# Kernel optimization log

Measured on AMD Instinct MI355X. Metric: run time of the kernel, lower is better.

Reference implementation:

```python
import jax, jax.numpy as jnp
import numpy as np

LORA_RANK = 16
LORA_ALPHA = 32
CHUNK_SIZE = 256
TTT_LR = 0.01
CLIP_THRESHOLD = 1.0
SCALING = LORA_ALPHA / LORA_RANK
LN_EPS = 1e-5


def setup_inputs() -> dict:
    key = jax.random.key(0)
    ks = jax.random.split(key, 5)
    B, S, K, H = 2, 8192, 1024, 1024
    x = jax.random.normal(ks[0], (B, S, K), dtype=jnp.float32)
    Wb = jax.random.normal(ks[1], (H, K), dtype=jnp.float32) / np.sqrt(K)
    init_A = jax.random.normal(ks[2], (H, LORA_RANK), dtype=jnp.float32) * 0.01
    init_B = jax.random.normal(ks[3], (LORA_RANK, K), dtype=jnp.float32) * 0.01
    ln_gamma = jnp.ones((K,), dtype=jnp.float32)
    ln_beta = jnp.zeros((K,), dtype=jnp.float32)
    Wp = jax.random.normal(ks[4], (H, K), dtype=jnp.float32) / np.sqrt(K)
    return {"x": x, "Wb": Wb, "init_A": init_A, "init_B": init_B,
            "ln_gamma": ln_gamma, "ln_beta": ln_beta, "Wp": Wp}


def _forward(x, Wb, init_A, init_B, ln_gamma, ln_beta, Wp):
    B_sz, Seq, k_dim = x.shape
    h_dim = Wb.shape[0]
    r = init_A.shape[1]
    nc = Seq // CHUNK_SIZE  # Seq chosen divisible; pad_len == 0

    base_out = x @ Wb.T  # [B, S, H]

    # --- target construction under no_grad: LayerNorm + left-shift ---
    xd = jax.lax.stop_gradient(x)
    mu = jnp.mean(xd, axis=-1, keepdims=True)
    var = jnp.mean((xd - mu) ** 2, axis=-1, keepdims=True)
    xn = (xd - mu) * jax.lax.rsqrt(var + LN_EPS) * ln_gamma + ln_beta
    shifted = jnp.pad(xn[:, 1:, :], ((0, 0), (0, 1), (0, 0)))
    shifted = jax.lax.stop_gradient(shifted)

    V = shifted @ Wp.T  # [B, S, H]

    Z = x.reshape(B_sz * nc, CHUNK_SIZE, k_dim)
    Vc = V.reshape(B_sz * nc, CHUNK_SIZE, h_dim)

    # per-chunk fast-weight deltas
    proj_in = Z @ init_B.T                                # [BC, C, r]
    dA = jnp.einsum('bch,bcr->bhr', Vc, proj_in)          # [BC, H, r]
    proj_err = Vc @ init_A                                # [BC, C, r]
    dB = jnp.einsum('bcr,bck->brk', proj_err, Z)          # [BC, r, K]

    dA = dA.reshape(B_sz, nc, h_dim, r)
    dB = dB.reshape(B_sz, nc, r, k_dim)

    # exclusive cross-chunk cumsum
    accA = jnp.cumsum(dA, axis=1)
    accB = jnp.cumsum(dB, axis=1)
    accA = jnp.concatenate([jnp.zeros_like(accA[:, :1]), accA[:, :-1]], axis=1)
    accB = jnp.concatenate([jnp.zeros_like(accB[:, :1]), accB[:, :-1]], axis=1)

    lr = TTT_LR * SCALING
    rawA = (lr * accA).reshape(-1, h_dim, r)
    rawB = (lr * accB).reshape(-1, r, k_dim)

    # joint norm clip (norm_type=2)
    norm_sq = (jnp.sum(rawA.astype(jnp.float32) ** 2, axis=(-2, -1), keepdims=True)
               + jnp.sum(rawB.astype(jnp.float32) ** 2, axis=(-2, -1), keepdims=True))
    total_norm = jnp.sqrt(norm_sq)
    coef = jnp.minimum(CLIP_THRESHOLD / (total_norm + 1e-6), 1.0).astype(rawA.dtype)

    A_eff = init_A[None] - rawA * coef  # [BC, H, r]
    B_eff = init_B[None] - rawB * coef  # [BC, r, K]

    mid = jnp.einsum('bck,brk->bcr', Z, B_eff)          # [BC, C, r]
    lora = jnp.einsum('bcr,bhr->bch', mid, A_eff)       # [BC, C, H]
    lora = lora.reshape(B_sz, Seq, h_dim)

    return base_out + lora * SCALING


def reference(x, Wb, init_A, init_B, ln_gamma, ln_beta, Wp):
    return _forward(x, Wb, init_A, init_B, ln_gamma, ln_beta, Wp)
```

## Files before the change

### kernel.cpp

```cpp
#include <hip/hip_runtime.h>

typedef __attribute__((ext_vector_type(8))) short s16x8;
typedef __attribute__((ext_vector_type(4))) float f32x4;
typedef unsigned short u16;

#define B_SZ 2
#define SEQ 8192
#define KD 1024
#define HD 1024
#define RK 16
#define CH 256
#define NCH 64
static constexpr float LR_SC = 0.02f;
static constexpr float SCALE_OUT = 2.0f;

__device__ __forceinline__ u16 f2b(float f) {
  union { float f; unsigned int u; } c; c.f = f;
  unsigned int u = c.u;
  unsigned int r = (u + 0x7fffu + ((u >> 16) & 1u)) >> 16;
  return (u16)r;
}
__device__ __forceinline__ float b2f(u16 v) {
  union { unsigned int u; float f; } c; c.u = ((unsigned int)v) << 16; return c.f;
}
__device__ __forceinline__ void async16(const u16* g, u16* l) {
  __builtin_amdgcn_global_load_lds((const __attribute__((address_space(1))) void*)g,
                                   (__attribute__((address_space(3))) void*)l, 16, 0, 0);
}

__global__ __launch_bounds__(256) void cvt_bf16(const float* __restrict__ src,
                                                u16* __restrict__ dst, int n) {
  int i = (blockIdx.x * 256 + threadIdx.x) * 4;
  if (i < n) {
    float4 v = *(const float4*)(src + i);
    ushort4 o; o.x = f2b(v.x); o.y = f2b(v.y); o.z = f2b(v.z); o.w = f2b(v.w);
    *(ushort4*)(dst + i) = o;
  }
}

__global__ __launch_bounds__(256) void cvt_at(const float* __restrict__ A,
                                              u16* __restrict__ At) {
  int i = blockIdx.x * 256 + threadIdx.x;
  if (i < HD * RK) {
    int h = i >> 4, j = i & 15;
    At[(size_t)j * HD + h] = f2b(A[i]);
  }
}

__global__ __launch_bounds__(256) void ln_shift(const float* __restrict__ x,
                                                const float* __restrict__ gamma,
                                                const float* __restrict__ beta,
                                                u16* __restrict__ xb,
                                                u16* __restrict__ shb) {
  int row = blockIdx.x;
  int t = threadIdx.x;
  int s = row & (SEQ - 1);
  const float* xr = x + (size_t)row * KD;
  float4 v = *(const float4*)(xr + t * 4);
  ushort4 o; o.x = f2b(v.x); o.y = f2b(v.y); o.z = f2b(v.z); o.w = f2b(v.w);
  *(ushort4*)(xb + (size_t)row * KD + t * 4) = o;

  if (s == 0) {
    ushort4 z; z.x = 0; z.y = 0; z.z = 0; z.w = 0;
    *(ushort4*)(shb + ((size_t)row + SEQ - 1) * KD + t * 4) = z;
    return;
  }
  float s1 = v.x + v.y + v.z + v.w;
  float s2 = v.x * v.x + v.y * v.y + v.z * v.z + v.w * v.w;
  #pragma unroll
  for (int off = 32; off > 0; off >>= 1) {
    s1 += __shfl_down(s1, off);
    s2 += __shfl_down(s2, off);
  }
  __shared__ float red[8];
  int wave = t >> 6, lane = t & 63;
  if (lane == 0) { red[wave * 2] = s1; red[wave * 2 + 1] = s2; }
  __syncthreads();
  float sum = red[0] + red[2] + red[4] + red[6];
  float ssq = red[1] + red[3] + red[5] + red[7];
  float mu = sum * (1.0f / KD);
  float var = ssq * (1.0f / KD) - mu * mu;
  float rstd = rsqrtf(var + 1e-5f);
  float4 g = *(const float4*)(gamma + t * 4);
  float4 bb = *(const float4*)(beta + t * 4);
  ushort4 so;
  so.x = f2b((v.x - mu) * rstd * g.x + bb.x);
  so.y = f2b((v.y - mu) * rstd * g.y + bb.y);
  so.z = f2b((v.z - mu) * rstd * g.z + bb.z);
  so.w = f2b((v.w - mu) * rstd * g.w + bb.w);
  *(ushort4*)(shb + (size_t)(row - 1) * KD + t * 4) = so;
}

__global__ __launch_bounds__(256, 2) void gemm_v(const u16* __restrict__ A,
                                                 const u16* __restrict__ Bm,
                                                 u16* __restrict__ C) {
  constexpr int BM = 128, BN = 128, BK = 32, N = HD, Kd = KD;
  __shared__ u16 As[BM * BK];
  __shared__ u16 Bs[BN * BK];
  int tid = threadIdx.x;
  int lane = tid & 63, wave = tid >> 6;
  int m0 = blockIdx.y * BM, n0 = blockIdx.x * BN;
  int wm = (wave >> 1) * 64, wn = (wave & 1) * 64;
  int lr = lane & 15, lk = (lane >> 4) * 8;
  f32x4 acc[4][4] = {};

  const u16* gbase; u16* lbase;
  if (wave < 2) { gbase = A + (size_t)(m0 + wave * 64) * Kd; lbase = As + wave * 64 * BK; }
  else          { gbase = Bm + (size_t)(n0 + (wave - 2) * 64) * Kd; lbase = Bs + (wave - 2) * 64 * BK; }
  int srow = lane >> 2, scol = (lane & 3) * 8;
  const u16* gsrc = gbase + (size_t)srow * Kd + scol;

  for (int k0 = 0; k0 < Kd; k0 += BK) {
    #pragma unroll
    for (int i = 0; i < 4; i++)
      async16(gsrc + (size_t)i * 16 * Kd, lbase + i * 16 * BK);
    gsrc += BK;
    __syncthreads();
    s16x8 af[4], bfr[4];
    #pragma unroll
    for (int i = 0; i < 4; i++) af[i] = *(const s16x8*)(As + (wm + i * 16 + lr) * BK + lk);
    #pragma unroll
    for (int j = 0; j < 4; j++) bfr[j] = *(const s16x8*)(Bs + (wn + j * 16 + lr) * BK + lk);
    #pragma unroll
    for (int i = 0; i < 4; i++)
      #pragma unroll
      for (int j = 0; j < 4; j++)
        acc[i][j] = __builtin_amdgcn_mfma_f32_16x16x32_bf16(af[i], bfr[j], acc[i][j], 0, 0, 0);
    __syncthreads();
  }
  int rb = (lane >> 4) * 4, cc = lane & 15;
  #pragma unroll
  for (int i = 0; i < 4; i++)
    #pragma unroll
    for (int j = 0; j < 4; j++)
      #pragma unroll
      for (int p = 0; p < 4; p++)
        C[(size_t)(m0 + wm + i * 16 + rb + p) * N + (n0 + wn + j * 16 + cc)] = f2b(acc[i][j][p]);
}

__global__ __launch_bounds__(256, 2) void gemm_fused(const u16* __restrict__ A,
                                                     const u16* __restrict__ Bm,
                                                     const u16* __restrict__ mid2,
                                                     const u16* __restrict__ Aef,
                                                     float* __restrict__ C) {
  constexpr int BM = 128, BN = 128, BK = 32, N = HD, Kd = KD;
  __shared__ u16 As[BM * BK];
  __shared__ u16 Bs[BN * BK];
  int tid = threadIdx.x;
  int lane = tid & 63, wave = tid >> 6;
  int m0 = blockIdx.y * BM, n0 = blockIdx.x * BN;
  int wm = (wave >> 1) * 64, wn = (wave & 1) * 64;
  int lr = lane & 15, lk = (lane >> 4) * 8;
  f32x4 acc[4][4] = {};

  const u16* gbase; u16* lbase;
  if (wave < 2) { gbase = A + (size_t)(m0 + wave * 64) * Kd; lbase = As + wave * 64 * BK; }
  else          { gbase = Bm + (size_t)(n0 + (wave - 2) * 64) * Kd; lbase = Bs + (wave - 2) * 64 * BK; }
  int srow = lane >> 2, scol = (lane & 3) * 8;
  const u16* gsrc = gbase + (size_t)srow * Kd + scol;

  for (int k0 = 0; k0 < Kd; k0 += BK) {
    #pragma unroll
    for (int i = 0; i < 4; i++)
      async16(gsrc + (size_t)i * 16 * Kd, lbase + i * 16 * BK);
    gsrc += BK;
    __syncthreads();
    s16x8 af[4], bfr[4];
    #pragma unroll
    for (int i = 0; i < 4; i++) af[i] = *(const s16x8*)(As + (wm + i * 16 + lr) * BK + lk);
    #pragma unroll
    for (int j = 0; j < 4; j++) bfr[j] = *(const s16x8*)(Bs + (wn + j * 16 + lr) * BK + lk);
    #pragma unroll
    for (int i = 0; i < 4; i++)
      #pragma unroll
      for (int j = 0; j < 4; j++)
        acc[i][j] = __builtin_amdgcn_mfma_f32_16x16x32_bf16(af[i], bfr[j], acc[i][j], 0, 0, 0);
    __syncthreads();
  }

  {
    int chunk = blockIdx.y >> 1;
    const u16* mbase = mid2;
    const u16* abase = Aef + (size_t)chunk * (HD * RK);
    int klane = lane >> 4;
    s16x8 am2[4], bn2[4];
    #pragma unroll
    for (int i = 0; i < 4; i++) {
      if (klane < 2)
        am2[i] = *(const s16x8*)(mbase + (size_t)(m0 + wm + i * 16 + lr) * RK + klane * 8);
      else { s16x8 z = {}; am2[i] = z; }
    }
    #pragma unroll
    for (int j = 0; j < 4; j++) {
      if (klane < 2)
        bn2[j] = *(const s16x8*)(abase + (size_t)(n0 + wn + j * 16 + lr) * RK + klane * 8);
      else { s16x8 z = {}; bn2[j] = z; }
    }
    #pragma unroll
    for (int i = 0; i < 4; i++)
      #pragma unroll
      for (int j = 0; j < 4; j++)
        acc[i][j] = __builtin_amdgcn_mfma_f32_16x16x32_bf16(am2[i], bn2[j], acc[i][j], 0, 0, 0);
  }

  int rb = (lane >> 4) * 4, cc = lane & 15;
  #pragma unroll
  for (int i = 0; i < 4; i++)
    #pragma unroll
    for (int j = 0; j < 4; j++)
      #pragma unroll
      for (int p = 0; p < 4; p++)
        C[(size_t)(m0 + wm + i * 16 + rb + p) * N + (n0 + wn + j * 16 + cc)] = acc[i][j][p];
}

__global__ __launch_bounds__(256) void rank16_proj(const u16* __restrict__ xb,
                                                   const u16* __restrict__ Vb,
                                                   const u16* __restrict__ iBb,
                                                   const u16* __restrict__ iAt,
                                                   float* __restrict__ pin,
                                                   float* __restrict__ per) {
  const u16* X; const u16* W; float* O;
  if (blockIdx.z == 0) { X = xb; W = iBb; O = pin; }
  else                 { X = Vb; W = iAt; O = per; }
  int wave = threadIdx.x >> 6, lane = threadIdx.x & 63;
  int m0 = (blockIdx.x * 4 + wave) * 16;
  int lr = lane & 15, lk = (lane >> 4) * 8;
  const u16* xp = X + (size_t)(m0 + lr) * KD + lk;
  const u16* wp = W + (size_t)lr * KD + lk;
  f32x4 acc = {};
  #pragma unroll 4
  for (int k0 = 0; k0 < KD; k0 += 32) {
    s16x8 a = *(const s16x8*)xp;
    s16x8 b = *(const s16x8*)wp;
    acc = __builtin_amdgcn_mfma_f32_16x16x32_bf16(a, b, acc, 0, 0, 0);
    xp += 32; wp += 32;
  }
  int rb = (lane >> 4) * 4, cc = lane & 15;
  #pragma unroll
  for (int p = 0; p < 4; p++)
    O[(size_t)(m0 + rb + p) * RK + cc] = acc[p];
}

__global__ __launch_bounds__(256) void rank16_mid(const u16* __restrict__ xb,
                                                  const u16* __restrict__ Bef,
                                                  u16* __restrict__ mid2) {
  int wave = threadIdx.x >> 6, lane = threadIdx.x & 63;
  int m0 = (blockIdx.x * 4 + wave) * 16;
  int chunk = m0 >> 8;
  int lr = lane & 15, lk = (lane >> 4) * 8;
  const u16* xp = xb + (size_t)(m0 + lr) * KD + lk;
  const u16* wp = Bef + (size_t)chunk * (RK * KD) + (size_t)lr * KD + lk;
  f32x4 acc = {};
  #pragma unroll 4
  for (int k0 = 0; k0 < KD; k0 += 32) {
    s16x8 a = *(const s16x8*)xp;
    s16x8 b = *(const s16x8*)wp;
    acc = __builtin_amdgcn_mfma_f32_16x16x32_bf16(a, b, acc, 0, 0, 0);
    xp += 32; wp += 32;
  }
  int rb = (lane >> 4) * 4, cc = lane & 15;
  #pragma unroll
  for (int p = 0; p < 4; p++)
    mid2[(size_t)(m0 + rb + p) * RK + cc] = f2b(SCALE_OUT * acc[p]);
}

__global__ __launch_bounds__(256) void dadb_kernel(const u16* __restrict__ xb,
                                                   const u16* __restrict__ Vb,
                                                   const float* __restrict__ proj_in,
                                                   const float* __restrict__ proj_err,
                                                   float* __restrict__ dA,
                                                   float* __restrict__ dB) {
  int tile = blockIdx.x;
  int chunk = blockIdx.y;
  int which = blockIdx.z;
  int t = threadIdx.x;
  __shared__ float P[CH * RK];
  const float* psrc = which ? proj_err : proj_in;
  for (int i = t; i < 1024; i += 256)
    *(float4*)&P[i * 4] = *(const float4*)&psrc[(size_t)chunk * 4096 + i * 4];
  __syncthreads();
  float acc[16];
  #pragma unroll
  for (int j = 0; j < 16; j++) acc[j] = 0.f;
  int col = tile * 256 + t;
  const u16* src = which ? (xb + (size_t)chunk * CH * KD + col)
                         : (Vb + (size_t)chunk * CH * HD + col);
  for (int c = 0; c < 256; c++) {
    float v = b2f(src[(size_t)c * 1024]);
    const float4* pr = (const float4*)&P[c * 16];
    #pragma unroll
    for (int q = 0; q < 4; q++) {
      float4 p = pr[q];
      acc[q*4+0] += v * p.x; acc[q*4+1] += v * p.y;
      acc[q*4+2] += v * p.z; acc[q*4+3] += v * p.w;
    }
  }
  if (which == 0) {
    float* o = dA + (size_t)chunk * 16384 + (size_t)col * 16;
    #pragma unroll
    for (int q = 0; q < 4; q++) {
      float4 r; r.x = acc[q*4]; r.y = acc[q*4+1]; r.z = acc[q*4+2]; r.w = acc[q*4+3];
      *(float4*)&o[q * 4] = r;
    }
  } else {
    float* o = dB + (size_t)chunk * 16384 + col;
    #pragma unroll
    for (int j = 0; j < 16; j++) o[(size_t)j * 1024] = acc[j];
  }
}

__global__ __launch_bounds__(256) void cumsum_kernel(const float* __restrict__ dA,
                                                     const float* __restrict__ dB,
                                                     float* __restrict__ rawA,
                                                     float* __restrict__ rawB) {
  int idx = blockIdx.x * 256 + threadIdx.x;
  int which = idx >> 15;
  int rem = idx & 32767;
  int b = rem >> 14;
  int e = rem & 16383;
  const float* src = which ? dB : dA;
  float* dst = which ? rawB : rawA;
  size_t base = (size_t)b * 32 * 16384 + e;
  float run = 0.f;
  for (int i = 0; i < 32; i++) {
    size_t off = base + (size_t)i * 16384;
    float nv = src[off];
    dst[off] = LR_SC * run;
    run += nv;
  }
}

__global__ __launch_bounds__(256) void coef_kernel(const float* __restrict__ rawA,
                                                   const float* __restrict__ rawB,
                                                   float* __restrict__ coef) {
  int chunk = blockIdx.x, t = threadIdx.x;
  const float* a = rawA + (size_t)chunk * 16384;
  const float* b = rawB + (size_t)chunk * 16384;
  float s = 0.f;
  for (int i = t * 4; i < 16384; i += 1024) {
    float4 v = *(const float4*)(a + i);
    s += v.x*v.x + v.y*v.y + v.z*v.z + v.w*v.w;
    float4 w = *(const float4*)(b + i);
    s += w.x*w.x + w.y*w.y + w.z*w.z + w.w*w.w;
  }
  #pragma unroll
  for (int off = 32; off > 0; off >>= 1) s += __shfl_down(s, off);
  __shared__ float red[4];
  int wave = t >> 6, lane = t & 63;
  if (lane == 0) red[wave] = s;
  __syncthreads();
  if (t == 0) {
    float tot = red[0] + red[1] + red[2] + red[3];
    float n = sqrtf(tot);
    coef[chunk] = fminf(1.0f / (n + 1e-6f), 1.0f);
  }
}

__global__ __launch_bounds__(256) void eff_kernel(const float* __restrict__ initA,
                                                  const float* __restrict__ initB,
                                                  const float* __restrict__ rawA,
                                                  const float* __restrict__ rawB,
                                                  const float* __restrict__ coef,
                                                  u16* __restrict__ Aef,
                                                  u16* __restrict__ Bef) {
  int idx = blockIdx.x * 256 + threadIdx.x;
  int which = idx >> 18;
  int rem = idx & 262143;
  int chunk = rem >> 12;
  int e = (rem & 4095) * 4;
  float cf = coef[chunk];
  const float* ini = which ? initB : initA;
  const float* raw = (which ? rawB : rawA) + (size_t)chunk * 16384;
  u16* out = (which ? Bef : Aef) + (size_t)chunk * 16384;
  float4 iv = *(const float4*)(ini + e);
  float4 rv = *(const float4*)(raw + e);
  ushort4 r;
  r.x = f2b(iv.x - rv.x * cf); r.y = f2b(iv.y - rv.y * cf);
  r.z = f2b(iv.z - rv.z * cf); r.w = f2b(iv.w - rv.w * cf);
  *(ushort4*)(out + e) = r;
}

extern "C" void kernel_launch(void* const* d_in, const int* in_sizes, int n_in,
                              void* d_out, int out_size, void* d_ws, size_t ws_size,
                              hipStream_t stream) {
  (void)in_sizes; (void)n_in; (void)out_size; (void)ws_size;
  const float* x     = (const float*)d_in[0];
  const float* Wb    = (const float*)d_in[1];
  const float* initA = (const float*)d_in[2];
  const float* initB = (const float*)d_in[3];
  const float* gamma = (const float*)d_in[4];
  const float* beta  = (const float*)d_in[5];
  const float* Wp    = (const float*)d_in[6];
  float* out = (float*)d_out;

  char* ws = (char*)d_ws;
  size_t off = 0;
  auto alloc = [&](size_t bytes) -> void* {
    void* p = ws + off;
    off = (off + bytes + 255) & ~(size_t)255;
    return p;
  };
  const size_t ROWS = (size_t)B_SZ * SEQ;
  u16* xb    = (u16*)alloc(ROWS * KD * 2);
  u16* shb   = (u16*)alloc(ROWS * KD * 2);
  u16* Wbb   = (u16*)alloc((size_t)HD * KD * 2);
  u16* Wpb   = (u16*)alloc((size_t)HD * KD * 2);
  u16* iBb   = (u16*)alloc((size_t)RK * KD * 2);
  u16* iAt   = (u16*)alloc((size_t)RK * HD * 2);
  u16* Vb    = (u16*)alloc(ROWS * HD * 2);
  float* pin = (float*)alloc((size_t)NCH * CH * RK * 4);
  float* per = (float*)alloc((size_t)NCH * CH * RK * 4);
  float* dA  = (float*)alloc((size_t)NCH * 16384 * 4);
  float* dB  = (float*)alloc((size_t)NCH * 16384 * 4);
  float* rawA= (float*)alloc((size_t)NCH * 16384 * 4);
  float* rawB= (float*)alloc((size_t)NCH * 16384 * 4);
  float* cf  = (float*)alloc(NCH * 4);
  u16* Aef   = (u16*)alloc((size_t)NCH * 16384 * 2);
  u16* Bef   = (u16*)alloc((size_t)NCH * 16384 * 2);
  u16* mid2  = (u16*)alloc(ROWS * RK * 2);

  cvt_bf16<<<1024, 256, 0, stream>>>(Wb, Wbb, HD * KD);
  cvt_bf16<<<1024, 256, 0, stream>>>(Wp, Wpb, HD * KD);
  cvt_bf16<<<16, 256, 0, stream>>>(initB, iBb, RK * KD);
  cvt_at<<<64, 256, 0, stream>>>(initA, iAt);
  ln_shift<<<ROWS, 256, 0, stream>>>(x, gamma, beta, xb, shb);
  gemm_v<<<dim3(HD / 128, ROWS / 128), 256, 0, stream>>>(shb, Wpb, Vb);
  rank16_proj<<<dim3(256, 1, 2), 256, 0, stream>>>(xb, Vb, iBb, iAt, pin, per);
  dadb_kernel<<<dim3(4, NCH, 2), 256, 0, stream>>>(xb, Vb, pin, per, dA, dB);
  cumsum_kernel<<<256, 256, 0, stream>>>(dA, dB, rawA, rawB);
  coef_kernel<<<NCH, 256, 0, stream>>>(rawA, rawB, cf);
  eff_kernel<<<2048, 256, 0, stream>>>(initA, initB, rawA, rawB, cf, Aef, Bef);
  rank16_mid<<<256, 256, 0, stream>>>(xb, Bef, mid2);
  gemm_fused<<<dim3(HD / 128, ROWS / 128), 256, 0, stream>>>(xb, Wbb, mid2, Aef, out);
}
```

Baseline: 315.8 us.

## Eliminate V GEMM by reassociating through Wp and swizzle LDS in fused GEMM

Drops the full S×H×K GEMM that built V. The rank-16 projections are reassociated instead: proj_err uses shifted @ (Wp^T initA), precomputed once, and dA is computed as Wp @ cumsum(shifted^T proj_in), using a small per-chunk MFMA GEMM after the cumsum. This removes roughly half of the large-GEMM FLOPs and the V write and read traffic. It adds a bf16 rounding of the cumulative G and of Wp·A, which changes numerics slightly. The fused output GEMM also gains an XOR swizzle on its LDS tiles to reduce bank conflicts.

```diff
diff --git a/kernel.cpp b/kernel.cpp
--- a/kernel.cpp
+++ b/kernel.cpp
@@ -38,13 +38,23 @@
   }
 }
 
-__global__ __launch_bounds__(256) void cvt_at(const float* __restrict__ A,
-                                              u16* __restrict__ At) {
-  int i = blockIdx.x * 256 + threadIdx.x;
-  if (i < HD * RK) {
-    int h = i >> 4, j = i & 15;
-    At[(size_t)j * HD + h] = f2b(A[i]);
-  }
+__global__ __launch_bounds__(256) void wpat_kernel(const float* __restrict__ initA,
+                                                   const float* __restrict__ Wp,
+                                                   u16* __restrict__ WpAT) {
+  int t = threadIdx.x;
+  int k = blockIdx.x * 64 + (t & 63);
+  int rq = t >> 6;
+  float a0 = 0.f, a1 = 0.f, a2 = 0.f, a3 = 0.f;
+  #pragma unroll 8
+  for (int h = 0; h < HD; h++) {
+    float w = Wp[(size_t)h * KD + k];
+    float4 a = *(const float4*)(initA + h * RK + rq * 4);
+    a0 += w * a.x; a1 += w * a.y; a2 += w * a.z; a3 += w * a.w;
+  }
+  WpAT[(size_t)(rq * 4 + 0) * KD + k] = f2b(a0);
+  WpAT[(size_t)(rq * 4 + 1) * KD + k] = f2b(a1);
+  WpAT[(size_t)(rq * 4 + 2) * KD + k] = f2b(a2);
+  WpAT[(size_t)(rq * 4 + 3) * KD + k] = f2b(a3);
 }
 
 __global__ __launch_bounds__(256) void ln_shift(const float* __restrict__ x,
@@ -91,53 +101,6 @@
   *(ushort4*)(shb + (size_t)(row - 1) * KD + t * 4) = so;
 }
 
-__global__ __launch_bounds__(256, 2) void gemm_v(const u16* __restrict__ A,
-                                                 const u16* __restrict__ Bm,
-                                                 u16* __restrict__ C) {
-  constexpr int BM = 128, BN = 128, BK = 32, N = HD, Kd = KD;
-  __shared__ u16 As[BM * BK];
-  __shared__ u16 Bs[BN * BK];
-  int tid = threadIdx.x;
-  int lane = tid & 63, wave = tid >> 6;
-  int m0 = blockIdx.y * BM, n0 = blockIdx.x * BN;
-  int wm = (wave >> 1) * 64, wn = (wave & 1) * 64;
-  int lr = lane & 15, lk = (lane >> 4) * 8;
-  f32x4 acc[4][4] = {};
-
-  const u16* gbase; u16* lbase;
-  if (wave < 2) { gbase = A + (size_t)(m0 + wave * 64) * Kd; lbase = As + wave * 64 * BK; }
-  else          { gbase = Bm + (size_t)(n0 + (wave - 2) * 64) * Kd; lbase = Bs + (wave - 2) * 64 * BK; }
-  int srow = lane >> 2, scol = (lane & 3) * 8;
-  const u16* gsrc = gbase + (size_t)srow * Kd + scol;
-
-  for (int k0 = 0; k0 < Kd; k0 += BK) {
-    #pragma unroll
-    for (int i = 0; i < 4; i++)
-      async16(gsrc + (size_t)i * 16 * Kd, lbase + i * 16 * BK);
-    gsrc += BK;
-    __syncthreads();
-    s16x8 af[4], bfr[4];
-    #pragma unroll
-    for (int i = 0; i < 4; i++) af[i] = *(const s16x8*)(As + (wm + i * 16 + lr) * BK + lk);
-    #pragma unroll
-    for (int j = 0; j < 4; j++) bfr[j] = *(const s16x8*)(Bs + (wn + j * 16 + lr) * BK + lk);
-    #pragma unroll
-    for (int i = 0; i < 4; i++)
-      #pragma unroll
-      for (int j = 0; j < 4; j++)
-        acc[i][j] = __builtin_amdgcn_mfma_f32_16x16x32_bf16(af[i], bfr[j], acc[i][j], 0, 0, 0);
-    __syncthreads();
-  }
-  int rb = (lane >> 4) * 4, cc = lane & 15;
-  #pragma unroll
-  for (int i = 0; i < 4; i++)
-    #pragma unroll
-    for (int j = 0; j < 4; j++)
-      #pragma unroll
-      for (int p = 0; p < 4; p++)
-        C[(size_t)(m0 + wm + i * 16 + rb + p) * N + (n0 + wn + j * 16 + cc)] = f2b(acc[i][j][p]);
-}
-
 __global__ __launch_bounds__(256, 2) void gemm_fused(const u16* __restrict__ A,
                                                      const u16* __restrict__ Bm,
                                                      const u16* __restrict__ mid2,
@@ -150,13 +113,15 @@
   int lane = tid & 63, wave = tid >> 6;
   int m0 = blockIdx.y * BM, n0 = blockIdx.x * BN;
   int wm = (wave >> 1) * 64, wn = (wave & 1) * 64;
-  int lr = lane & 15, lk = (lane >> 4) * 8;
+  int lr = lane & 15;
+  int swz = (((lane >> 4) ^ ((lr >> 1) & 3)) & 3) * 8;
   f32x4 acc[4][4] = {};
 
   const u16* gbase; u16* lbase;
   if (wave < 2) { gbase = A + (size_t)(m0 + wave * 64) * Kd; lbase = As + wave * 64 * BK; }
   else          { gbase = Bm + (size_t)(n0 + (wave - 2) * 64) * Kd; lbase = Bs + (wave - 2) * 64 * BK; }
-  int srow = lane >> 2, scol = (lane & 3) * 8;
+  int srow = lane >> 2;
+  int scol = (((lane & 3) ^ ((srow >> 1) & 3)) & 3) * 8;
   const u16* gsrc = gbase + (size_t)srow * Kd + scol;
 
   for (int k0 = 0; k0 < Kd; k0 += BK) {
@@ -167,9 +132,9 @@
     __syncthreads();
     s16x8 af[4], bfr[4];
     #pragma unroll
-    for (int i = 0; i < 4; i++) af[i] = *(const s16x8*)(As + (wm + i * 16 + lr) * BK + lk);
-    #pragma unroll
-    for (int j = 0; j < 4; j++) bfr[j] = *(const s16x8*)(Bs + (wn + j * 16 + lr) * BK + lk);
+    for (int i = 0; i < 4; i++) af[i] = *(const s16x8*)(As + (wm + i * 16 + lr) * BK + swz);
+    #pragma unroll
+    for (int j = 0; j < 4; j++) bfr[j] = *(const s16x8*)(Bs + (wn + j * 16 + lr) * BK + swz);
     #pragma unroll
     for (int i = 0; i < 4; i++)
       #pragma unroll
@@ -180,14 +145,13 @@
 
   {
     int chunk = blockIdx.y >> 1;
-    const u16* mbase = mid2;
     const u16* abase = Aef + (size_t)chunk * (HD * RK);
     int klane = lane >> 4;
     s16x8 am2[4], bn2[4];
     #pragma unroll
     for (int i = 0; i < 4; i++) {
       if (klane < 2)
-        am2[i] = *(const s16x8*)(mbase + (size_t)(m0 + wm + i * 16 + lr) * RK + klane * 8);
+        am2[i] = *(const s16x8*)(mid2 + (size_t)(m0 + wm + i * 16 + lr) * RK + klane * 8);
       else { s16x8 z = {}; am2[i] = z; }
     }
     #pragma unroll
@@ -214,14 +178,14 @@
 }
 
 __global__ __launch_bounds__(256) void rank16_proj(const u16* __restrict__ xb,
-                                                   const u16* __restrict__ Vb,
+                                                   const u16* __restrict__ shb,
                                                    const u16* __restrict__ iBb,
-                                                   const u16* __restrict__ iAt,
+                                                   const u16* __restrict__ WpAT,
                                                    float* __restrict__ pin,
                                                    float* __restrict__ per) {
   const u16* X; const u16* W; float* O;
   if (blockIdx.z == 0) { X = xb; W = iBb; O = pin; }
-  else                 { X = Vb; W = iAt; O = per; }
+  else                 { X = shb; W = WpAT; O = per; }
   int wave = threadIdx.x >> 6, lane = threadIdx.x & 63;
   int m0 = (blockIdx.x * 4 + wave) * 16;
   int lr = lane & 15, lk = (lane >> 4) * 8;
@@ -264,18 +228,18 @@
     mid2[(size_t)(m0 + rb + p) * RK + cc] = f2b(SCALE_OUT * acc[p]);
 }
 
-__global__ __launch_bounds__(256) void dadb_kernel(const u16* __restrict__ xb,
-                                                   const u16* __restrict__ Vb,
-                                                   const float* __restrict__ proj_in,
-                                                   const float* __restrict__ proj_err,
-                                                   float* __restrict__ dA,
-                                                   float* __restrict__ dB) {
+__global__ __launch_bounds__(256) void gk_kernel(const u16* __restrict__ xb,
+                                                 const u16* __restrict__ shb,
+                                                 const float* __restrict__ pin,
+                                                 const float* __restrict__ per,
+                                                 float* __restrict__ G,
+                                                 float* __restrict__ dB) {
   int tile = blockIdx.x;
   int chunk = blockIdx.y;
   int which = blockIdx.z;
   int t = threadIdx.x;
   __shared__ float P[CH * RK];
-  const float* psrc = which ? proj_err : proj_in;
+  const float* psrc = which ? per : pin;
   for (int i = t; i < 1024; i += 256)
     *(float4*)&P[i * 4] = *(const float4*)&psrc[(size_t)chunk * 4096 + i * 4];
   __syncthreads();
@@ -283,8 +247,7 @@
   #pragma unroll
   for (int j = 0; j < 16; j++) acc[j] = 0.f;
   int col = tile * 256 + t;
-  const u16* src = which ? (xb + (size_t)chunk * CH * KD + col)
-                         : (Vb + (size_t)chunk * CH * HD + col);
+  const u16* src = (which ? xb : shb) + (size_t)chunk * CH * KD + col;
   for (int c = 0; c < 256; c++) {
     float v = b2f(src[(size_t)c * 1024]);
     const float4* pr = (const float4*)&P[c * 16];
@@ -295,39 +258,61 @@
       acc[q*4+2] += v * p.z; acc[q*4+3] += v * p.w;
     }
   }
-  if (which == 0) {
-    float* o = dA + (size_t)chunk * 16384 + (size_t)col * 16;
-    #pragma unroll
-    for (int q = 0; q < 4; q++) {
-      float4 r; r.x = acc[q*4]; r.y = acc[q*4+1]; r.z = acc[q*4+2]; r.w = acc[q*4+3];
-      *(float4*)&o[q * 4] = r;
-    }
-  } else {
-    float* o = dB + (size_t)chunk * 16384 + col;
-    #pragma unroll
-    for (int j = 0; j < 16; j++) o[(size_t)j * 1024] = acc[j];
-  }
-}
-
-__global__ __launch_bounds__(256) void cumsum_kernel(const float* __restrict__ dA,
+  float* o = (which ? dB : G) + (size_t)chunk * 16384 + col;
+  #pragma unroll
+  for (int j = 0; j < 16; j++) o[(size_t)j * 1024] = acc[j];
+}
+
+__global__ __launch_bounds__(256) void cumsum_kernel(const float* __restrict__ G,
                                                      const float* __restrict__ dB,
-                                                     float* __restrict__ rawA,
+                                                     u16* __restrict__ rawG,
                                                      float* __restrict__ rawB) {
   int idx = blockIdx.x * 256 + threadIdx.x;
   int which = idx >> 15;
   int rem = idx & 32767;
   int b = rem >> 14;
   int e = rem & 16383;
-  const float* src = which ? dB : dA;
-  float* dst = which ? rawB : rawA;
   size_t base = (size_t)b * 32 * 16384 + e;
-  float run = 0.f;
-  for (int i = 0; i < 32; i++) {
-    size_t off = base + (size_t)i * 16384;
-    float nv = src[off];
-    dst[off] = LR_SC * run;
-    run += nv;
-  }
+  if (which == 0) {
+    float run = 0.f;
+    for (int i = 0; i < 32; i++) {
+      size_t off = base + (size_t)i * 16384;
+      float nv = G[off];
+      rawG[off] = f2b(LR_SC * run);
+      run += nv;
+    }
+  } else {
+    float run = 0.f;
+    for (int i = 0; i < 32; i++) {
+      size_t off = base + (size_t)i * 16384;
+      float nv = dB[off];
+      rawB[off] = LR_SC * run;
+      run += nv;
+    }
+  }
+}
+
+__global__ __launch_bounds__(256) void dagemm(const u16* __restrict__ Wpb,
+                                              const u16* __restrict__ rawG,
+                                              float* __restrict__ rawA) {
+  int wave = threadIdx.x >> 6, lane = threadIdx.x & 63;
+  int m0 = (blockIdx.x * 4 + wave) * 16;
+  int chunk = blockIdx.y;
+  int lr = lane & 15, lk = (lane >> 4) * 8;
+  const u16* ap = Wpb + (size_t)(m0 + lr) * KD + lk;
+  const u16* bp = rawG + (size_t)chunk * 16384 + (size_t)lr * KD + lk;
+  f32x4 acc = {};
+  #pragma unroll 4
+  for (int k0 = 0; k0 < KD; k0 += 32) {
+    s16x8 a = *(const s16x8*)ap;
+    s16x8 b = *(const s16x8*)bp;
+    acc = __builtin_amdgcn_mfma_f32_16x16x32_bf16(a, b, acc, 0, 0, 0);
+    ap += 32; bp += 32;
+  }
+  int rb = (lane >> 4) * 4, cc = lane & 15;
+  #pragma unroll
+  for (int p = 0; p < 4; p++)
+    rawA[(size_t)chunk * 16384 + (size_t)(m0 + rb + p) * RK + cc] = acc[p];
 }
 
 __global__ __launch_bounds__(256) void coef_kernel(const float* __restrict__ rawA,
@@ -406,14 +391,14 @@
   u16* Wbb   = (u16*)alloc((size_t)HD * KD * 2);
   u16* Wpb   = (u16*)alloc((size_t)HD * KD * 2);
   u16* iBb   = (u16*)alloc((size_t)RK * KD * 2);
-  u16* iAt   = (u16*)alloc((size_t)RK * HD * 2);
-  u16* Vb    = (u16*)alloc(ROWS * HD * 2);
+  u16* WpAT  = (u16*)alloc((size_t)RK * KD * 2);
   float* pin = (float*)alloc((size_t)NCH * CH * RK * 4);
   float* per = (float*)alloc((size_t)NCH * CH * RK * 4);
-  float* dA  = (float*)alloc((size_t)NCH * 16384 * 4);
+  float* G   = (float*)alloc((size_t)NCH * 16384 * 4);
   float* dB  = (float*)alloc((size_t)NCH * 16384 * 4);
+  u16* rawG  = (u16*)alloc((size_t)NCH * 16384 * 2);
+  float* rawB= (float*)alloc((size_t)NCH * 16384 * 4);
   float* rawA= (float*)alloc((size_t)NCH * 16384 * 4);
-  float* rawB= (float*)alloc((size_t)NCH * 16384 * 4);
   float* cf  = (float*)alloc(NCH * 4);
   u16* Aef   = (u16*)alloc((size_t)NCH * 16384 * 2);
   u16* Bef   = (u16*)alloc((size_t)NCH * 16384 * 2);
@@ -422,12 +407,12 @@
   cvt_bf16<<<1024, 256, 0, stream>>>(Wb, Wbb, HD * KD);
   cvt_bf16<<<1024, 256, 0, stream>>>(Wp, Wpb, HD * KD);
   cvt_bf16<<<16, 256, 0, stream>>>(initB, iBb, RK * KD);
-  cvt_at<<<64, 256, 0, stream>>>(initA, iAt);
+  wpat_kernel<<<16, 256, 0, stream>>>(initA, Wp, WpAT);
   ln_shift<<<ROWS, 256, 0, stream>>>(x, gamma, beta, xb, shb);
-  gemm_v<<<dim3(HD / 128, ROWS / 128), 256, 0, stream>>>(shb, Wpb, Vb);
-  rank16_proj<<<dim3(256, 1, 2), 256, 0, stream>>>(xb, Vb, iBb, iAt, pin, per);
-  dadb_kernel<<<dim3(4, NCH, 2), 256, 0, stream>>>(xb, Vb, pin, per, dA, dB);
-  cumsum_kernel<<<256, 256, 0, stream>>>(dA, dB, rawA, rawB);
+  rank16_proj<<<dim3(256, 1, 2), 256, 0, stream>>>(xb, shb, iBb, WpAT, pin, per);
+  gk_kernel<<<dim3(4, NCH, 2), 256, 0, stream>>>(xb, shb, pin, per, G, dB);
+  cumsum_kernel<<<256, 256, 0, stream>>>(G, dB, rawG, rawB);
+  dagemm<<<dim3(16, NCH), 256, 0, stream>>>(Wpb, rawG, rawA);
   coef_kernel<<<NCH, 256, 0, stream>>>(rawA, rawB, cf);
   eff_kernel<<<2048, 256, 0, stream>>>(initA, initB, rawA, rawB, cf, Aef, Bef);
   rank16_mid<<<256, 256, 0, stream>>>(xb, Bef, mid2);
```

Result: slower. 365.9 us (+15.9%).
